# Optimization experiments

Measured on AMD Instinct MI355X. Metric: run time of the kernel, lower is better.

## Reference

```python
import jax, jax.numpy as jnp
import numpy as np

BS, L, D = 1, 2048, 4096  # L = hidden_size (seq len after permute), D = feature channels (loop count)


def setup_inputs() -> dict:
    key = jax.random.key(0)
    k1, k2, k3 = jax.random.split(key, 3)
    tokens_to_embrace_bs = jax.random.normal(k1, (BS, L, D), dtype=jnp.float32)
    W_in = 0.02 * jax.random.normal(k2, (L, L), dtype=jnp.float32)      # linear_in weight [out,in]
    W_out = 0.02 * jax.random.normal(k3, (L, 2 * L), dtype=jnp.float32)  # linear_out weight [out,in]
    return {"tokens_to_embrace_bs": tokens_to_embrace_bs, "W_in": W_in, "W_out": W_out}


def reference(tokens_to_embrace_bs, W_in, W_out):
    # context: [bs, D, L] -- each of the D feature channels is a length-L query
    context = jnp.transpose(tokens_to_embrace_bs, (0, 2, 1))
    # Fused version of the per-channel Python loop: all D queries at once.
    Q = jnp.einsum('bdl,ml->bdm', context, W_in)        # linear_in on every query -> [bs,D,L]
    S = jnp.einsum('bql,bkl->bqk', Q, context)          # attention scores [bs,D,D]
    A = jax.nn.softmax(S, axis=-1)                      # attention weights
    mix = jnp.einsum('bqk,bkl->bql', A, context)        # [bs,D,L]
    comb = jnp.concatenate([mix, Q], axis=-1)           # [bs,D,2L]
    out = jnp.tanh(jnp.einsum('bdc,lc->bdl', comb, W_out))  # attention output per channel [bs,D,L]
    # accumulate over the D loop iterations -> [bs,1,L] (bs=1, so broadcast add is exact)
    scores = out.sum(axis=1, keepdims=True)
    scores = scores / scores.max()
    scores = jax.nn.softmax(scores, axis=-1)
    return scores.squeeze()  # [L]
```

## Files before the change

### kernel.cpp

```cpp
#include <hip/hip_runtime.h>
#include <hip/hip_bf16.h>
#include <math.h>


typedef __attribute__((ext_vector_type(8))) short short8;
typedef __attribute__((ext_vector_type(4))) float f32x4;

__device__ __forceinline__ unsigned short f2bf(float f) {
  unsigned u = __float_as_uint(f);
  return (unsigned short)((u + 0x7FFF + ((u >> 16) & 1)) >> 16);
}

typedef const __attribute__((address_space(1))) unsigned int* gas_t;
typedef __attribute__((address_space(3))) unsigned int* las_t;
__device__ __forceinline__ void dma16(const unsigned short* g, unsigned short* l)
{
  __builtin_amdgcn_global_load_lds((gas_t)(const void*)g, (las_t)(void*)l,
                                   16, 0, 0);
}

__global__ __launch_bounds__(512, 2) void gemm256(
    const unsigned short* __restrict__ A, const unsigned short* __restrict__ B,
    float* __restrict__ C, int K, int lda, int ldb, int ldc)
{
  __shared__ unsigned short sm[2][2][256 * 64];
  const int t = threadIdx.x;
  const int lane = t & 63;
  const int wid = t >> 6;
  const int wr = wid >> 2;
  const int wc = wid & 3;
  const int lr = lane & 15, lq = lane >> 4;

  int bx, by;
  {
    int wg = blockIdx.x;
    int x = wg & 7, s = wg >> 3;
    by = (x & 3) * 4 + (s >> 3);
    bx = (x >> 2) * 8 + (s & 7);
  }
  const int i0 = by * 256, j0 = bx * 256;

  const int r_ = t >> 3;
  const int ss_ = ((t & 7) ^ (r_ & 7)) * 8;

  auto issue = [&](int buf, int c, int k0) {
    const unsigned short* M;
    int ld, r0;
    if (c < 4) { M = A; ld = lda; r0 = i0 + (c & 3) * 64; }
    else       { M = B; ld = ldb; r0 = j0 + (c & 3) * 64; }
    unsigned short* lb = &sm[buf][c >> 2][(c & 3) * 4096];
    dma16(M + (size_t)(r0 + r_) * ld + k0 + ss_, lb + wid * 512);
  };

  auto frag = [&](const unsigned short* mat, int row, int kh) -> short8 {
    int lb = row * 128 + kh * 64 + (lq << 4);
    int pb = lb ^ ((row & 7) << 4);
    return *(const short8*)((const char*)mat + pb);
  };

  f32x4 acc[8][4];
  #pragma unroll
  for (int a = 0; a < 8; a++)
    #pragma unroll
    for (int b = 0; b < 4; b++) acc[a][b] = (f32x4){0.f, 0.f, 0.f, 0.f};

  issue(0, 0, 0); issue(0, 2, 0);
  issue(0, 4, 0); issue(0, 5, 0);
  issue(0, 6, 0); issue(0, 7, 0);
  issue(0, 1, 0); issue(0, 3, 0);
  asm volatile("s_waitcnt vmcnt(2)" ::: "memory");
  __builtin_amdgcn_s_barrier();

  const int NT = K >> 6;
  for (int kt = 0; kt < NT; kt++) {
    const int cur = kt & 1;
    const unsigned short* As = sm[cur][0];
    const unsigned short* Bs = sm[cur][1];
    const int kn = (kt + 1) << 6;
    const bool st = (kt + 1 < NT);
    short8 bfr[4][2];

    #pragma unroll
    for (int p = 0; p < 4; p++) {
      short8 a0k0 = frag(As, wr * 128 + (p * 2 + 0) * 16 + lr, 0);
      short8 a0k1 = frag(As, wr * 128 + (p * 2 + 0) * 16 + lr, 1);
      short8 a1k0 = frag(As, wr * 128 + (p * 2 + 1) * 16 + lr, 0);
      short8 a1k1 = frag(As, wr * 128 + (p * 2 + 1) * 16 + lr, 1);
      if (p == 0) {
        #pragma unroll
        for (int nf = 0; nf < 4; nf++) {
          bfr[nf][0] = frag(Bs, wc * 64 + nf * 16 + lr, 0);
          bfr[nf][1] = frag(Bs, wc * 64 + nf * 16 + lr, 1);
        }
      }
      if (st) {
        if (p == 0) { issue(cur ^ 1, 0, kn); issue(cur ^ 1, 2, kn); }
        if (p == 1) { issue(cur ^ 1, 4, kn); issue(cur ^ 1, 5, kn); }
        if (p == 2) { issue(cur ^ 1, 6, kn); issue(cur ^ 1, 7, kn); }
        if (p == 3) { issue(cur ^ 1, 1, kn); issue(cur ^ 1, 3, kn); }
      }
      asm volatile("" ::: "memory");
      __builtin_amdgcn_s_barrier();
      __builtin_amdgcn_s_setprio(1);
      #pragma unroll
      for (int nf = 0; nf < 4; nf++) {
        acc[p * 2 + 0][nf] = __builtin_amdgcn_mfma_f32_16x16x32_bf16(
            a0k0, bfr[nf][0], acc[p * 2 + 0][nf], 0, 0, 0);
        acc[p * 2 + 0][nf] = __builtin_amdgcn_mfma_f32_16x16x32_bf16(
            a0k1, bfr[nf][1], acc[p * 2 + 0][nf], 0, 0, 0);
        acc[p * 2 + 1][nf] = __builtin_amdgcn_mfma_f32_16x16x32_bf16(
            a1k0, bfr[nf][0], acc[p * 2 + 1][nf], 0, 0, 0);
        acc[p * 2 + 1][nf] = __builtin_amdgcn_mfma_f32_16x16x32_bf16(
            a1k1, bfr[nf][1], acc[p * 2 + 1][nf], 0, 0, 0);
      }
      __builtin_amdgcn_s_setprio(0);
      if (p == 1) {
        if (st) asm volatile("s_waitcnt vmcnt(4)" ::: "memory");
        else    asm volatile("s_waitcnt vmcnt(0)" ::: "memory");
      }
      if (p == 3 && st) asm volatile("s_waitcnt vmcnt(2)" ::: "memory");
      asm volatile("" ::: "memory");
      __builtin_amdgcn_s_barrier();
    }
  }

  #pragma unroll
  for (int mf = 0; mf < 8; mf++)
    #pragma unroll
    for (int nf = 0; nf < 4; nf++)
      #pragma unroll
      for (int r = 0; r < 4; r++) {
        int row = i0 + wr * 128 + mf * 16 + lq * 4 + r;
        int col = j0 + wc * 64 + nf * 16 + lr;
        C[(size_t)row * ldc + col] = acc[mf][nf][r];
      }
}

template<int CMODE>
__global__ __launch_bounds__(512, 2) void gemm_n128(
    const unsigned short* __restrict__ A, const unsigned short* __restrict__ B,
    void* __restrict__ Cv, float* __restrict__ colsum,
    int K, int lda, int ldb, int ldc)
{
  __shared__ unsigned short sm[3][384 * 64];
  const int t = threadIdx.x;
  const int lane = t & 63, wid = t >> 6;
  const int wr = wid >> 2;
  const int wc = wid & 3;
  const int lr = lane & 15, lq = lane >> 4;

  int bx, by;
  {
    int wg = blockIdx.x;
    int x = wg & 7, s = wg >> 3;
    by = (x & 3) * 4 + (s >> 3);
    bx = (x >> 2) * 8 + (s & 7);
  }
  const int i0 = by * 256, j0 = bx * 128;

  const int r_ = t >> 3;
  const int ss_ = ((t & 7) ^ (r_ & 7)) * 8;

  auto issue = [&](int buf, int c, int k0) {
    const unsigned short* M;
    int ld, r0;
    if (c < 4) { M = A; ld = lda; r0 = i0 + c * 64; }
    else       { M = B; ld = ldb; r0 = j0 + (c - 4) * 64; }
    unsigned short* lb = &sm[buf][c * 4096];
    dma16(M + (size_t)(r0 + r_) * ld + k0 + ss_, lb + wid * 512);
  };

  auto frag = [&](const unsigned short* mat, int row, int kh) -> short8 {
    int lb = row * 128 + kh * 64 + (lq << 4);
    int pb = lb ^ ((row & 7) << 4);
    return *(const short8*)((const char*)mat + pb);
  };

  f32x4 acc[8][2];
  #pragma unroll
  for (int a = 0; a < 8; a++)
    #pragma unroll
    for (int b = 0; b < 2; b++) acc[a][b] = (f32x4){0.f, 0.f, 0.f, 0.f};

  #pragma unroll
  for (int c = 0; c < 6; c++) issue(0, c, 0);
  #pragma unroll
  for (int c = 0; c < 6; c++) issue(1, c, 64);
  asm volatile("s_waitcnt vmcnt(6)" ::: "memory");
  __builtin_amdgcn_s_barrier();

  const int NT = K >> 6;
  int cur = 0;
  for (int kt = 0; kt < NT; kt++) {
    const unsigned short* As = sm[cur];
    const unsigned short* Bs = sm[cur] + 256 * 64;
    const int b2 = (cur + 2 >= 3) ? cur - 1 : cur + 2;
    const int kn = (kt + 2) << 6;
    const bool st = (kt + 2 < NT);

    short8 af[4][2], bfr[2][2];
    #pragma unroll
    for (int m = 0; m < 4; m++) {
      af[m][0] = frag(As, wr * 128 + m * 16 + lr, 0);
      af[m][1] = frag(As, wr * 128 + m * 16 + lr, 1);
    }
    #pragma unroll
    for (int n = 0; n < 2; n++) {
      bfr[n][0] = frag(Bs, wc * 32 + n * 16 + lr, 0);
      bfr[n][1] = frag(Bs, wc * 32 + n * 16 + lr, 1);
    }
    if (st) {
      issue(b2, 0, kn); issue(b2, 2, kn);
      issue(b2, 4, kn); issue(b2, 5, kn);
    }
    __builtin_amdgcn_s_setprio(1);
    #pragma unroll
    for (int m = 0; m < 4; m++)
      #pragma unroll
      for (int n = 0; n < 2; n++) {
        acc[m][n] = __builtin_amdgcn_mfma_f32_16x16x32_bf16(
            af[m][0], bfr[n][0], acc[m][n], 0, 0, 0);
        acc[m][n] = __builtin_amdgcn_mfma_f32_16x16x32_bf16(
            af[m][1], bfr[n][1], acc[m][n], 0, 0, 0);
      }
    __builtin_amdgcn_s_setprio(0);

    #pragma unroll
    for (int m = 0; m < 4; m++) {
      af[m][0] = frag(As, wr * 128 + (4 + m) * 16 + lr, 0);
      af[m][1] = frag(As, wr * 128 + (4 + m) * 16 + lr, 1);
    }
    if (st) { issue(b2, 1, kn); issue(b2, 3, kn); }
    __builtin_amdgcn_s_setprio(1);
    #pragma unroll
    for (int m = 0; m < 4; m++)
      #pragma unroll
      for (int n = 0; n < 2; n++) {
        acc[4 + m][n] = __builtin_amdgcn_mfma_f32_16x16x32_bf16(
            af[m][0], bfr[n][0], acc[4 + m][n], 0, 0, 0);
        acc[4 + m][n] = __builtin_amdgcn_mfma_f32_16x16x32_bf16(
            af[m][1], bfr[n][1], acc[4 + m][n], 0, 0, 0);
      }
    __builtin_amdgcn_s_setprio(0);

    if (kt + 1 < NT) {
      if (st) asm volatile("s_waitcnt vmcnt(6)" ::: "memory");
      else    asm volatile("s_waitcnt vmcnt(0)" ::: "memory");
      __builtin_amdgcn_s_barrier();
    }
    cur = (cur + 1 == 3) ? 0 : cur + 1;
  }

  if (CMODE == 2) {
    #pragma unroll
    for (int n = 0; n < 2; n++) {
      float s = 0.f;
      #pragma unroll
      for (int m = 0; m < 8; m++)
        #pragma unroll
        for (int r = 0; r < 4; r++) s += tanhf(acc[m][n][r]);
      s += __shfl_xor(s, 16);
      s += __shfl_xor(s, 32);
      if (lq == 0) atomicAdd(&colsum[j0 + wc * 32 + n * 16 + lr], s);
    }
  } else {
    #pragma unroll
    for (int m = 0; m < 8; m++)
      #pragma unroll
      for (int n = 0; n < 2; n++)
        #pragma unroll
        for (int r = 0; r < 4; r++) {
          int row = i0 + wr * 128 + m * 16 + lq * 4 + r;
          int col = j0 + wc * 32 + n * 16 + lr;
          ((unsigned short*)Cv)[(size_t)row * ldc + col] = f2bf(acc[m][n][r]);
        }
  }
}

template<int BF32, int CMODE>
__global__ __launch_bounds__(256) void mfma_gemm(
    const unsigned short* __restrict__ Abf, const void* __restrict__ Bv,
    void* __restrict__ Cv, float* __restrict__ colsum,
    int K, int lda, int ldb, int ldc)
{
  __shared__ unsigned short As[128 * 32];
  __shared__ unsigned short Bs[128 * 32];
  const int t = threadIdx.x;
  const int lane = t & 63, wid = t >> 6;
  const int wm = (wid >> 1) * 64, wn = (wid & 1) * 64;
  const int i0 = blockIdx.y * 128, j0 = blockIdx.x * 128;
  const int lr = lane & 15, lq = lane >> 4;

  f32x4 acc[4][4];
  #pragma unroll
  for (int a = 0; a < 4; a++)
    #pragma unroll
    for (int b = 0; b < 4; b++) acc[a][b] = (f32x4){0.f, 0.f, 0.f, 0.f};

  for (int k0 = 0; k0 < K; k0 += 32) {
    #pragma unroll
    for (int u = 0; u < 2; u++) {
      int vid = u * 256 + t;
      int row = vid >> 2, kq = (vid & 3) * 8;
      dma16(Abf + (size_t)(i0 + row) * lda + k0 + kq,
            &As[(u * 256 + wid * 64) * 8]);
    }
    if (BF32 == 0) {
      #pragma unroll
      for (int u = 0; u < 2; u++) {
        int vid = u * 256 + t;
        int row = vid >> 2, kq = (vid & 3) * 8;
        dma16((const unsigned short*)Bv + (size_t)(j0 + row) * ldb + k0 + kq,
              &Bs[(u * 256 + wid * 64) * 8]);
      }
    } else {
      #pragma unroll
      for (int u = 0; u < 2; u++) {
        int vid = u * 256 + t;
        int row = vid >> 2, kq = (vid & 3) * 8;
        const float* s = (const float*)Bv + (size_t)(j0 + row) * ldb + k0 + kq;
        float4 f0 = *(const float4*)s;
        float4 f1 = *(const float4*)(s + 4);
        union { unsigned short h[8]; int4 v; } pk;
        pk.h[0] = f2bf(f0.x); pk.h[1] = f2bf(f0.y);
        pk.h[2] = f2bf(f0.z); pk.h[3] = f2bf(f0.w);
        pk.h[4] = f2bf(f1.x); pk.h[5] = f2bf(f1.y);
        pk.h[6] = f2bf(f1.z); pk.h[7] = f2bf(f1.w);
        *(int4*)&Bs[(size_t)vid * 8] = pk.v;
      }
    }
    __syncthreads();

    short8 af[4], bfr[4];
    #pragma unroll
    for (int tm = 0; tm < 4; tm++)
      af[tm] = *(const short8*)&As[(wm + tm * 16 + lr) * 32 + lq * 8];
    #pragma unroll
    for (int tn = 0; tn < 4; tn++)
      bfr[tn] = *(const short8*)&Bs[(wn + tn * 16 + lr) * 32 + lq * 8];

    #pragma unroll
    for (int tm = 0; tm < 4; tm++)
      #pragma unroll
      for (int tn = 0; tn < 4; tn++)
        acc[tm][tn] = __builtin_amdgcn_mfma_f32_16x16x32_bf16(
            af[tm], bfr[tn], acc[tm][tn], 0, 0, 0);
    __syncthreads();
  }

  if (CMODE == 2) {
    #pragma unroll
    for (int tn = 0; tn < 4; tn++) {
      float s = 0.f;
      #pragma unroll
      for (int tm = 0; tm < 4; tm++)
        #pragma unroll
        for (int r = 0; r < 4; r++) s += tanhf(acc[tm][tn][r]);
      s += __shfl_xor(s, 16);
      s += __shfl_xor(s, 32);
      if (lq == 0) atomicAdd(&colsum[j0 + wn + tn * 16 + lr], s);
    }
  } else {
    #pragma unroll
    for (int tm = 0; tm < 4; tm++)
      #pragma unroll
      for (int tn = 0; tn < 4; tn++)
        #pragma unroll
        for (int r = 0; r < 4; r++) {
          int row = i0 + wm + tm * 16 + lq * 4 + r;
          int col = j0 + wn + tn * 16 + lr;
          if (CMODE == 0)
            ((float*)Cv)[(size_t)row * ldc + col] = acc[tm][tn][r];
          else
            ((unsigned short*)Cv)[(size_t)row * ldc + col] = f2bf(acc[tm][tn][r]);
        }
  }
}

__global__ __launch_bounds__(256) void transpose_bf16(
    const float* __restrict__ T, unsigned short* __restrict__ Tt)
{
  __shared__ float tile[64][65];
  const int tx = threadIdx.x & 63;
  const int ty = threadIdx.x >> 6;
  const int k0 = blockIdx.x * 64;
  const int l0 = blockIdx.y * 64;
  #pragma unroll
  for (int u = 0; u < 16; u++) {
    int row = ty * 16 + u;
    tile[row][tx] = T[(size_t)(l0 + row) * 4096 + k0 + tx];
  }
  __syncthreads();
  #pragma unroll
  for (int u = 0; u < 16; u++) {
    int row = ty * 16 + u;
    Tt[(size_t)(k0 + row) * 2048 + l0 + tx] = f2bf(tile[tx][row]);
  }
}

__global__ __launch_bounds__(256) void cvt_bf16(
    const float* __restrict__ in, unsigned short* __restrict__ out, int n8)
{
  int i = blockIdx.x * 256 + threadIdx.x;
  if (i >= n8) return;
  float4 f0 = ((const float4*)in)[(size_t)i * 2];
  float4 f1 = ((const float4*)in)[(size_t)i * 2 + 1];
  union { unsigned short h[8]; int4 v; } pk;
  pk.h[0] = f2bf(f0.x); pk.h[1] = f2bf(f0.y);
  pk.h[2] = f2bf(f0.z); pk.h[3] = f2bf(f0.w);
  pk.h[4] = f2bf(f1.x); pk.h[5] = f2bf(f1.y);
  pk.h[6] = f2bf(f1.z); pk.h[7] = f2bf(f1.w);
  ((int4*)out)[i] = pk.v;
}

__global__ __launch_bounds__(256) void softmax_bf16(float* __restrict__ S)
{
  float* p = S + (size_t)blockIdx.x * 4096;
  const int tid = threadIdx.x;
  float4 v[4];
  #pragma unroll
  for (int u = 0; u < 4; u++) v[u] = ((const float4*)p)[tid * 4 + u];

  float m = -3.4e38f;
  #pragma unroll
  for (int u = 0; u < 4; u++)
    m = fmaxf(m, fmaxf(fmaxf(v[u].x, v[u].y), fmaxf(v[u].z, v[u].w)));
  #pragma unroll
  for (int off = 32; off > 0; off >>= 1) m = fmaxf(m, __shfl_down(m, off, 64));
  __shared__ float redm[4];
  if ((tid & 63) == 0) redm[tid >> 6] = m;
  __syncthreads();
  m = fmaxf(fmaxf(redm[0], redm[1]), fmaxf(redm[2], redm[3]));

  float s = 0.f;
  #pragma unroll
  for (int u = 0; u < 4; u++) {
    v[u].x = __expf(v[u].x - m); v[u].y = __expf(v[u].y - m);
    v[u].z = __expf(v[u].z - m); v[u].w = __expf(v[u].w - m);
    s += v[u].x + v[u].y + v[u].z + v[u].w;
  }
  #pragma unroll
  for (int off = 32; off > 0; off >>= 1) s += __shfl_down(s, off, 64);
  __shared__ float reds[4];
  if ((tid & 63) == 0) reds[tid >> 6] = s;
  __syncthreads();
  s = reds[0] + reds[1] + reds[2] + reds[3];
  const float inv = 1.f / s;

  unsigned short* a = (unsigned short*)p;
  #pragma unroll
  for (int h = 0; h < 2; h++) {
    union { unsigned short u[8]; int4 q; } pk;
    #pragma unroll
    for (int j = 0; j < 2; j++) {
      float4 w = v[h * 2 + j];
      pk.u[j * 4 + 0] = f2bf(w.x * inv); pk.u[j * 4 + 1] = f2bf(w.y * inv);
      pk.u[j * 4 + 2] = f2bf(w.z * inv); pk.u[j * 4 + 3] = f2bf(w.w * inv);
    }
    ((int4*)a)[tid * 2 + h] = pk.q;
  }
}

__global__ void zero_k(float* p, int n)
{
  int i = blockIdx.x * 256 + threadIdx.x;
  if (i < n) p[i] = 0.f;
}

__global__ __launch_bounds__(256) void finalize_k(const float* __restrict__ scores,
                                                  float* __restrict__ out)
{
  const int tid = threadIdx.x;
  float s[8];
  #pragma unroll
  for (int u = 0; u < 8; u++) s[u] = scores[tid + u * 256];

  __shared__ float red[4];

  float m = -3.4e38f;
  #pragma unroll
  for (int u = 0; u < 8; u++) m = fmaxf(m, s[u]);
  #pragma unroll
  for (int off = 32; off > 0; off >>= 1) m = fmaxf(m, __shfl_down(m, off, 64));
  if ((tid & 63) == 0) red[tid >> 6] = m;
  __syncthreads();
  m = fmaxf(fmaxf(red[0], red[1]), fmaxf(red[2], red[3]));
  __syncthreads();

  const float inv1 = 1.f / m;
  #pragma unroll
  for (int u = 0; u < 8; u++) s[u] *= inv1;

  float m2 = -3.4e38f;
  #pragma unroll
  for (int u = 0; u < 8; u++) m2 = fmaxf(m2, s[u]);
  #pragma unroll
  for (int off = 32; off > 0; off >>= 1) m2 = fmaxf(m2, __shfl_down(m2, off, 64));
  if ((tid & 63) == 0) red[tid >> 6] = m2;
  __syncthreads();
  m2 = fmaxf(fmaxf(red[0], red[1]), fmaxf(red[2], red[3]));
  __syncthreads();

  float sum = 0.f;
  #pragma unroll
  for (int u = 0; u < 8; u++) { s[u] = expf(s[u] - m2); sum += s[u]; }
  #pragma unroll
  for (int off = 32; off > 0; off >>= 1) sum += __shfl_down(sum, off, 64);
  if ((tid & 63) == 0) red[tid >> 6] = sum;
  __syncthreads();
  sum = red[0] + red[1] + red[2] + red[3];

  const float invs = 1.f / sum;
  #pragma unroll
  for (int u = 0; u < 8; u++)
    out[tid + u * 256] = s[u] * invs;
}

extern "C" void kernel_launch(void* const* d_in, const int* in_sizes, int n_in,
                              void* d_out, int out_size, void* d_ws, size_t ws_size,
                              hipStream_t stream)
{
  const float* T    = (const float*)d_in[0];
  const float* Win  = (const float*)d_in[1];
  const float* Wout = (const float*)d_in[2];
  float* out = (float*)d_out;

  const size_t FIX1 = 92274688ull + 16384;
  int R = 1024; bool pre = false;
  if      (ws_size >= FIX1 + (size_t)4096 * 16384) { pre = true; R = 4096; }
  else if (ws_size >= FIX1 + (size_t)2048 * 16384) { pre = true; R = 2048; }
  else if (ws_size >= FIX1 + (size_t)1024 * 16384) { pre = true; R = 1024; }

  unsigned short* Tt = (unsigned short*)d_ws;

  if (pre) {
    unsigned short* Tb    = Tt + (size_t)4096 * 2048;
    unsigned short* Winb  = Tb + (size_t)2048 * 4096;
    unsigned short* Woutb = Winb + (size_t)2048 * 2048;
    unsigned short* comb  = Woutb + (size_t)2048 * 4096;
    float* S      = (float*)(comb + (size_t)4096 * 4096);
    float* scores = S + (size_t)R * 4096;

    zero_k<<<8, 256, 0, stream>>>(scores, 2048);
    transpose_bf16<<<dim3(64, 32), 256, 0, stream>>>(T, Tt);
    cvt_bf16<<<4096, 256, 0, stream>>>(T, Tb, 1048576);
    cvt_bf16<<<2048, 256, 0, stream>>>(Win, Winb, 524288);
    cvt_bf16<<<4096, 256, 0, stream>>>(Wout, Woutb, 1048576);

    gemm_n128<1><<<256, 512, 0, stream>>>(
        Tt, Winb, comb + 2048, nullptr, 2048, 2048, 2048, 4096);
    for (int c = 0; c < 4096 / R; c++) {
      const size_t d0 = (size_t)c * R;
      if (R == 4096) {
        gemm256<<<256, 512, 0, stream>>>(
            comb + 2048, Tt, S, 2048, 4096, 2048, 4096);
      } else {
        mfma_gemm<0, 0><<<dim3(32, R / 128), 256, 0, stream>>>(
            comb + d0 * 4096 + 2048, Tt, S, nullptr, 2048, 4096, 2048, 4096);
      }
      softmax_bf16<<<R, 256, 0, stream>>>(S);
      if (R == 4096) {
        gemm_n128<1><<<256, 512, 0, stream>>>(
            (unsigned short*)S, Tb, comb, nullptr, 4096, 8192, 4096, 4096);
      } else {
        mfma_gemm<0, 1><<<dim3(16, R / 128), 256, 0, stream>>>(
            (unsigned short*)S, Tb, comb + d0 * 4096, nullptr, 4096, 8192, 4096, 4096);
      }
    }
    gemm_n128<2><<<256, 512, 0, stream>>>(
        comb, Woutb, nullptr, scores, 4096, 4096, 4096, 4096);
    finalize_k<<<1, 256, 0, stream>>>(scores, out);
  } else {
    unsigned short* comb = Tt + (size_t)4096 * 2048;
    float* S      = (float*)(comb + (size_t)4096 * 4096);
    float* scores = S + (size_t)1024 * 4096;

    zero_k<<<8, 256, 0, stream>>>(scores, 2048);
    transpose_bf16<<<dim3(64, 32), 256, 0, stream>>>(T, Tt);

    mfma_gemm<1, 1><<<dim3(16, 32), 256, 0, stream>>>(
        Tt, Win, comb + 2048, nullptr, 2048, 2048, 2048, 4096);
    for (int c = 0; c < 4; c++) {
      const size_t d0 = (size_t)c * 1024;
      mfma_gemm<0, 0><<<dim3(32, 8), 256, 0, stream>>>(
          comb + d0 * 4096 + 2048, Tt, S, nullptr, 2048, 4096, 2048, 4096);
      softmax_bf16<<<1024, 256, 0, stream>>>(S);
      mfma_gemm<1, 1><<<dim3(16, 8), 256, 0, stream>>>(
          (unsigned short*)S, T, comb + d0 * 4096, nullptr, 4096, 8192, 4096, 4096);
    }
    mfma_gemm<1, 2><<<dim3(16, 32), 256, 0, stream>>>(
        comb, Wout, nullptr, scores, 4096, 4096, 4096, 4096);
    finalize_k<<<1, 256, 0, stream>>>(scores, out);
  }
}
```

Before: 371.8 us.

## Replace 256x256 score GEMM with 256x128 kernel and fuse transpose with bf16 cast

The dedicated 256x256-tile score GEMM is removed, and the S = Q·Tᵀ product now runs on the 256x128 gemm_n128 kernel with a new fp32-output mode and a 512-block grid. The block-to-tile swizzle is generalized to derive an XCD-strided index from gridDim and a template column-count shift. The separate transpose and bf16-conversion passes over the input are fused into one kernel that reads T once and writes both layouts. This aims to improve load balance across CUs and cut one full read of the input tensor, at the cost of smaller tiles with lower per-block reuse in the score GEMM.

```diff
diff --git a/kernel.cpp b/kernel.cpp
--- a/kernel.cpp
+++ b/kernel.cpp
@@ -19,124 +19,7 @@
                                    16, 0, 0);
 }
 
-__global__ __launch_bounds__(512, 2) void gemm256(
-    const unsigned short* __restrict__ A, const unsigned short* __restrict__ B,
-    float* __restrict__ C, int K, int lda, int ldb, int ldc)
-{
-  __shared__ unsigned short sm[2][2][256 * 64];
-  const int t = threadIdx.x;
-  const int lane = t & 63;
-  const int wid = t >> 6;
-  const int wr = wid >> 2;
-  const int wc = wid & 3;
-  const int lr = lane & 15, lq = lane >> 4;
-
-  int bx, by;
-  {
-    int wg = blockIdx.x;
-    int x = wg & 7, s = wg >> 3;
-    by = (x & 3) * 4 + (s >> 3);
-    bx = (x >> 2) * 8 + (s & 7);
-  }
-  const int i0 = by * 256, j0 = bx * 256;
-
-  const int r_ = t >> 3;
-  const int ss_ = ((t & 7) ^ (r_ & 7)) * 8;
-
-  auto issue = [&](int buf, int c, int k0) {
-    const unsigned short* M;
-    int ld, r0;
-    if (c < 4) { M = A; ld = lda; r0 = i0 + (c & 3) * 64; }
-    else       { M = B; ld = ldb; r0 = j0 + (c & 3) * 64; }
-    unsigned short* lb = &sm[buf][c >> 2][(c & 3) * 4096];
-    dma16(M + (size_t)(r0 + r_) * ld + k0 + ss_, lb + wid * 512);
-  };
-
-  auto frag = [&](const unsigned short* mat, int row, int kh) -> short8 {
-    int lb = row * 128 + kh * 64 + (lq << 4);
-    int pb = lb ^ ((row & 7) << 4);
-    return *(const short8*)((const char*)mat + pb);
-  };
-
-  f32x4 acc[8][4];
-  #pragma unroll
-  for (int a = 0; a < 8; a++)
-    #pragma unroll
-    for (int b = 0; b < 4; b++) acc[a][b] = (f32x4){0.f, 0.f, 0.f, 0.f};
-
-  issue(0, 0, 0); issue(0, 2, 0);
-  issue(0, 4, 0); issue(0, 5, 0);
-  issue(0, 6, 0); issue(0, 7, 0);
-  issue(0, 1, 0); issue(0, 3, 0);
-  asm volatile("s_waitcnt vmcnt(2)" ::: "memory");
-  __builtin_amdgcn_s_barrier();
-
-  const int NT = K >> 6;
-  for (int kt = 0; kt < NT; kt++) {
-    const int cur = kt & 1;
-    const unsigned short* As = sm[cur][0];
-    const unsigned short* Bs = sm[cur][1];
-    const int kn = (kt + 1) << 6;
-    const bool st = (kt + 1 < NT);
-    short8 bfr[4][2];
-
-    #pragma unroll
-    for (int p = 0; p < 4; p++) {
-      short8 a0k0 = frag(As, wr * 128 + (p * 2 + 0) * 16 + lr, 0);
-      short8 a0k1 = frag(As, wr * 128 + (p * 2 + 0) * 16 + lr, 1);
-      short8 a1k0 = frag(As, wr * 128 + (p * 2 + 1) * 16 + lr, 0);
-      short8 a1k1 = frag(As, wr * 128 + (p * 2 + 1) * 16 + lr, 1);
-      if (p == 0) {
-        #pragma unroll
-        for (int nf = 0; nf < 4; nf++) {
-          bfr[nf][0] = frag(Bs, wc * 64 + nf * 16 + lr, 0);
-          bfr[nf][1] = frag(Bs, wc * 64 + nf * 16 + lr, 1);
-        }
-      }
-      if (st) {
-        if (p == 0) { issue(cur ^ 1, 0, kn); issue(cur ^ 1, 2, kn); }
-        if (p == 1) { issue(cur ^ 1, 4, kn); issue(cur ^ 1, 5, kn); }
-        if (p == 2) { issue(cur ^ 1, 6, kn); issue(cur ^ 1, 7, kn); }
-        if (p == 3) { issue(cur ^ 1, 1, kn); issue(cur ^ 1, 3, kn); }
-      }
-      asm volatile("" ::: "memory");
-      __builtin_amdgcn_s_barrier();
-      __builtin_amdgcn_s_setprio(1);
-      #pragma unroll
-      for (int nf = 0; nf < 4; nf++) {
-        acc[p * 2 + 0][nf] = __builtin_amdgcn_mfma_f32_16x16x32_bf16(
-            a0k0, bfr[nf][0], acc[p * 2 + 0][nf], 0, 0, 0);
-        acc[p * 2 + 0][nf] = __builtin_amdgcn_mfma_f32_16x16x32_bf16(
-            a0k1, bfr[nf][1], acc[p * 2 + 0][nf], 0, 0, 0);
-        acc[p * 2 + 1][nf] = __builtin_amdgcn_mfma_f32_16x16x32_bf16(
-            a1k0, bfr[nf][0], acc[p * 2 + 1][nf], 0, 0, 0);
-        acc[p * 2 + 1][nf] = __builtin_amdgcn_mfma_f32_16x16x32_bf16(
-            a1k1, bfr[nf][1], acc[p * 2 + 1][nf], 0, 0, 0);
-      }
-      __builtin_amdgcn_s_setprio(0);
-      if (p == 1) {
-        if (st) asm volatile("s_waitcnt vmcnt(4)" ::: "memory");
-        else    asm volatile("s_waitcnt vmcnt(0)" ::: "memory");
-      }
-      if (p == 3 && st) asm volatile("s_waitcnt vmcnt(2)" ::: "memory");
-      asm volatile("" ::: "memory");
-      __builtin_amdgcn_s_barrier();
-    }
-  }
-
-  #pragma unroll
-  for (int mf = 0; mf < 8; mf++)
-    #pragma unroll
-    for (int nf = 0; nf < 4; nf++)
-      #pragma unroll
-      for (int r = 0; r < 4; r++) {
-        int row = i0 + wr * 128 + mf * 16 + lq * 4 + r;
-        int col = j0 + wc * 64 + nf * 16 + lr;
-        C[(size_t)row * ldc + col] = acc[mf][nf][r];
-      }
-}
-
-template<int CMODE>
+template<int CMODE, int NXBS>
 __global__ __launch_bounds__(512, 2) void gemm_n128(
     const unsigned short* __restrict__ A, const unsigned short* __restrict__ B,
     void* __restrict__ Cv, float* __restrict__ colsum,
@@ -152,9 +35,10 @@
   int bx, by;
   {
     int wg = blockIdx.x;
-    int x = wg & 7, s = wg >> 3;
-    by = (x & 3) * 4 + (s >> 3);
-    bx = (x >> 2) * 8 + (s & 7);
+    int q = (int)gridDim.x >> 3;
+    int wgid = (wg & 7) * q + (wg >> 3);
+    by = wgid >> NXBS;
+    bx = wgid & ((1 << NXBS) - 1);
   }
   const int i0 = by * 256, j0 = bx * 128;
 
@@ -272,7 +156,10 @@
         for (int r = 0; r < 4; r++) {
           int row = i0 + wr * 128 + m * 16 + lq * 4 + r;
           int col = j0 + wc * 32 + n * 16 + lr;
-          ((unsigned short*)Cv)[(size_t)row * ldc + col] = f2bf(acc[m][n][r]);
+          if (CMODE == 0)
+            ((float*)Cv)[(size_t)row * ldc + col] = acc[m][n][r];
+          else
+            ((unsigned short*)Cv)[(size_t)row * ldc + col] = f2bf(acc[m][n][r]);
         }
   }
 }
@@ -377,6 +264,30 @@
   }
 }
 
+__global__ __launch_bounds__(256) void transpose_cvt_bf16(
+    const float* __restrict__ T, unsigned short* __restrict__ Tt,
+    unsigned short* __restrict__ Tb)
+{
+  __shared__ float tile[64][65];
+  const int tx = threadIdx.x & 63;
+  const int ty = threadIdx.x >> 6;
+  const int k0 = blockIdx.x * 64;
+  const int l0 = blockIdx.y * 64;
+  #pragma unroll
+  for (int u = 0; u < 16; u++) {
+    int row = ty * 16 + u;
+    float v = T[(size_t)(l0 + row) * 4096 + k0 + tx];
+    tile[row][tx] = v;
+    Tb[(size_t)(l0 + row) * 4096 + k0 + tx] = f2bf(v);
+  }
+  __syncthreads();
+  #pragma unroll
+  for (int u = 0; u < 16; u++) {
+    int row = ty * 16 + u;
+    Tt[(size_t)(k0 + row) * 2048 + l0 + tx] = f2bf(tile[tx][row]);
+  }
+}
+
 __global__ __launch_bounds__(256) void transpose_bf16(
     const float* __restrict__ T, unsigned short* __restrict__ Tt)
 {
@@ -542,32 +453,31 @@
     float* scores = S + (size_t)R * 4096;
 
     zero_k<<<8, 256, 0, stream>>>(scores, 2048);
-    transpose_bf16<<<dim3(64, 32), 256, 0, stream>>>(T, Tt);
-    cvt_bf16<<<4096, 256, 0, stream>>>(T, Tb, 1048576);
+    transpose_cvt_bf16<<<dim3(64, 32), 256, 0, stream>>>(T, Tt, Tb);
     cvt_bf16<<<2048, 256, 0, stream>>>(Win, Winb, 524288);
     cvt_bf16<<<4096, 256, 0, stream>>>(Wout, Woutb, 1048576);
 
-    gemm_n128<1><<<256, 512, 0, stream>>>(
+    gemm_n128<1, 4><<<256, 512, 0, stream>>>(
         Tt, Winb, comb + 2048, nullptr, 2048, 2048, 2048, 4096);
     for (int c = 0; c < 4096 / R; c++) {
       const size_t d0 = (size_t)c * R;
       if (R == 4096) {
-        gemm256<<<256, 512, 0, stream>>>(
-            comb + 2048, Tt, S, 2048, 4096, 2048, 4096);
+        gemm_n128<0, 5><<<512, 512, 0, stream>>>(
+            comb + 2048, Tt, S, nullptr, 2048, 4096, 2048, 4096);
       } else {
         mfma_gemm<0, 0><<<dim3(32, R / 128), 256, 0, stream>>>(
             comb + d0 * 4096 + 2048, Tt, S, nullptr, 2048, 4096, 2048, 4096);
       }
       softmax_bf16<<<R, 256, 0, stream>>>(S);
       if (R == 4096) {
-        gemm_n128<1><<<256, 512, 0, stream>>>(
+        gemm_n128<1, 4><<<256, 512, 0, stream>>>(
             (unsigned short*)S, Tb, comb, nullptr, 4096, 8192, 4096, 4096);
       } else {
         mfma_gemm<0, 1><<<dim3(16, R / 128), 256, 0, stream>>>(
             (unsigned short*)S, Tb, comb + d0 * 4096, nullptr, 4096, 8192, 4096, 4096);
       }
     }
-    gemm_n128<2><<<256, 512, 0, stream>>>(
+    gemm_n128<2, 4><<<256, 512, 0, stream>>>(
         comb, Woutb, nullptr, scores, 4096, 4096, 4096, 4096);
     finalize_k<<<1, 256, 0, stream>>>(scores, out);
   } else {
```

Result: no change. 371.2 us (-0.2%).
